# Optimization experiments

Hardware: AMD Instinct MI355X
Metric: run time of the kernel (lower is better)

The kernel has to match this reference:

```python
import jax, jax.numpy as jnp
import numpy as np

EPS = 1e-12

def l2norm(x):
    return x / jnp.maximum(jnp.linalg.norm(x, axis=-1, keepdims=True), EPS)

def setup_inputs() -> dict:
    key = jax.random.key(0)
    ks = jax.random.split(key, 10)
    B, N, Din, D, P, C = 2, 32768, 768, 512, 16, 2
    return {
        "x_s": jax.random.normal(ks[0], (B, N, Din), jnp.float32),
        "coord_s": jax.random.uniform(ks[1], (B, N, 2), jnp.float32),
        "x_l": jax.random.normal(ks[2], (B, N, Din), jnp.float32),
        "coord_l": jax.random.uniform(ks[3], (B, N, 2), jnp.float32),
        "W_proj": jax.random.normal(ks[4], (Din, D), jnp.float32) / np.sqrt(Din),
        "b_proj": jax.random.normal(ks[5], (D,), jnp.float32) * 0.01,
        "prototypes": jax.random.normal(ks[6], (P, D), jnp.float32),
        "text_low": l2norm(jax.random.normal(ks[7], (C, D), jnp.float32)),
        "text_high": l2norm(jax.random.normal(ks[8], (C, D), jnp.float32)),
        "label": jax.random.randint(ks[9], (B,), 0, C, jnp.int64),
    }

def forward_project(x, W, b):
    # Linear projection to hidden size, then L2 normalize (matches visual.forward_project + F.normalize)
    return l2norm(jnp.einsum('bni,id->bnd', x, W) + b)

def attention_pool(feats, prototypes):
    # feats: [B,N,D], prototypes: [P,D]
    D = feats.shape[-1]
    p = l2norm(prototypes)
    scores = jnp.einsum('bnd,pd->bpn', feats, p) / jnp.sqrt(jnp.asarray(D, feats.dtype))
    w = jax.nn.softmax(scores, axis=-1)                  # [B,P,N]
    attended = jnp.einsum('bpn,bnd->bpd', w, feats)       # [B,P,D]
    return l2norm(attended.mean(axis=1))                  # [B,D]

def reference(x_s, coord_s, x_l, coord_l, W_proj, b_proj, prototypes, text_low, text_high, label):
    x_s_proj = forward_project(x_s, W_proj, b_proj)
    x_l_proj = forward_project(x_l, W_proj, b_proj)
    feat_low = attention_pool(x_s_proj, prototypes)
    feat_high = attention_pool(x_l_proj, prototypes)
    logits = feat_low @ text_low.T + feat_high @ text_high.T   # [B,C]
    logp = jax.nn.log_softmax(logits, axis=-1)
    loss = -jnp.mean(jnp.take_along_axis(logp, label[:, None], axis=1))
    Y_prob = jax.nn.softmax(logits, axis=1)
    Y_hat = jnp.argmax(Y_prob, axis=1)
    return Y_prob, Y_hat, loss
```

## Files before the change

### kernel.cpp

```cpp
#include <hip/hip_runtime.h>
#include <hip/hip_bf16.h>
#include <math.h>

#define BB   2
#define NN   32768
#define DIN  768
#define DD   512
#define PP   16
#define MTOT (BB*NN)
#define MALL (2*MTOT)
#define NCHUNK 128
#define CHUNK  (NN/NCHUNK)
#define SCALE_INV_SQRT_D 0.04419417382415922f

typedef unsigned short u16;
typedef __attribute__((ext_vector_type(8))) short bf16x8;
typedef __attribute__((ext_vector_type(4))) float f32x4;

#define MFMA(a,b,c) __builtin_amdgcn_mfma_f32_16x16x32_bf16((a),(b),(c),0,0,0)

__device__ __forceinline__ unsigned pack2bf(float a, float b) {
  union { float f; unsigned u; } x{a}, y{b};
  unsigned ra = (x.u + 0x7FFFu + ((x.u >> 16) & 1u)) >> 16;
  unsigned rb = (y.u + 0x7FFFu + ((y.u >> 16) & 1u)) >> 16;
  return ra | (rb << 16);
}
__device__ __forceinline__ unsigned cvt2(float a, float b) {
  union { __hip_bfloat162 h; unsigned u; } x;
  x.h = __float22bfloat162_rn(make_float2(a, b));
  return x.u;
}
__device__ __forceinline__ u16 f2bf(float a) {
  union { float f; unsigned u; } x{a};
  return (u16)((x.u + 0x7FFFu + ((x.u >> 16) & 1u)) >> 16);
}
__device__ __forceinline__ float bf2f(u16 u) {
  union { unsigned u; float f; } x; x.u = ((unsigned)u) << 16; return x.f;
}

__device__ __forceinline__ float block_reduce_sum_256(float v, float* sred) {
  #pragma unroll
  for (int off = 32; off; off >>= 1) v += __shfl_down(v, off);
  const int lane = threadIdx.x & 63, w = threadIdx.x >> 6;
  if (lane == 0) sred[w] = v;
  __syncthreads();
  float r = sred[0] + sred[1] + sred[2] + sred[3];
  __syncthreads();
  return r;
}

__global__ __launch_bounds__(64) void pre_kernel(
    const float* __restrict__ W, const float* __restrict__ prot,
    uint4* __restrict__ Bf, uint4* __restrict__ pnb) {
  const int bid = blockIdx.x;
  const int lane = threadIdx.x;
  if (bid < 768) {
    const int nf = bid / 24, ks = bid % 24;
    const int n = nf*16 + (lane & 15);
    const int kb = ks*32 + (lane >> 4)*8;
    unsigned r0 = pack2bf(W[(size_t)(kb+0)*DD + n], W[(size_t)(kb+1)*DD + n]);
    unsigned r1 = pack2bf(W[(size_t)(kb+2)*DD + n], W[(size_t)(kb+3)*DD + n]);
    unsigned r2 = pack2bf(W[(size_t)(kb+4)*DD + n], W[(size_t)(kb+5)*DD + n]);
    unsigned r3 = pack2bf(W[(size_t)(kb+6)*DD + n], W[(size_t)(kb+7)*DD + n]);
    Bf[(size_t)bid*64 + lane] = make_uint4(r0, r1, r2, r3);
    return;
  }
  const int ks = bid - 768;
  const int p = lane & 15, seg = lane >> 4;
  float ssq = 0.f;
  for (int d = seg*128; d < seg*128 + 128; d += 4) {
    float4 v = *(const float4*)&prot[p*DD + d];
    ssq += v.x*v.x + v.y*v.y + v.z*v.z + v.w*v.w;
  }
  ssq += __shfl_xor(ssq, 16);
  ssq += __shfl_xor(ssq, 32);
  const float rnp = 1.f / fmaxf(sqrtf(ssq), 1e-12f);
  const int kb = ks*32 + seg*8;
  float v[8];
  #pragma unroll
  for (int j = 0; j < 8; ++j) v[j] = prot[p*DD + kb + j] * rnp;
  pnb[ks*64 + lane] = make_uint4(pack2bf(v[0],v[1]), pack2bf(v[2],v[3]),
                                 pack2bf(v[4],v[5]), pack2bf(v[6],v[7]));
}

__global__ __launch_bounds__(1024, 4) void gemm_kernel(
    const float* __restrict__ Xs, const float* __restrict__ Xl,
    const uint4* __restrict__ Bf, const float* __restrict__ bias,
    u16* __restrict__ proj, float* __restrict__ rnormb) {
  __shared__ __align__(16) unsigned char lds[163840];
  const int t = threadIdx.x, lane = t & 63, wid = t >> 6;
  const int wm = wid >> 3, wn = wid & 7;
  const int cl = lane & 15, cg = lane >> 4;
  const int m0g = blockIdx.x * 128;
  const float* Xb = (m0g < MTOT) ? Xs : Xl;
  const int m0l = m0g & (MTOT - 1);
  const int r = t >> 3, k8g = (t & 7) * 8;
  const float* gA = Xb + (size_t)(m0l + r) * DIN + k8g;
  const int aksl = k8g >> 5, acg = (k8g >> 3) & 3;
  const int awoff = ((r >> 4) * 2 + aksl) * 1024 + acg * 256
                  + (((r & 15) ^ ((acg << 1) | aksl)) << 4);

  f32x4 acc[4][4] = {};

#define STAGE_B(ktx, buf) \
  { _Pragma("unroll") \
    for (int q_ = 0; q_ < 4; ++q_) { \
      const int c_ = q_*16 + wid; \
      const uint4* src_ = Bf + ((size_t)((c_>>1)*24 + (ktx)*2 + (c_&1)))*64 + lane; \
      __builtin_amdgcn_global_load_lds( \
          (const __attribute__((address_space(1))) void*)src_, \
          (__attribute__((address_space(3))) void*)(lds + 32768 + (buf)*65536 + c_*1024 + lane*16), \
          16, 0, 0); \
    } }

  {
    STAGE_B(0, 0);
    float4 a0 = *(const float4*)gA;
    float4 a1 = *(const float4*)(gA + 4);
    *(uint4*)(lds + awoff) = make_uint4(cvt2(a0.x,a0.y), cvt2(a0.z,a0.w),
                                        cvt2(a1.x,a1.y), cvt2(a1.z,a1.w));
    __syncthreads();
  }
  for (int kt = 0; kt < 12; ++kt) {
    const int cur = kt & 1;
    float4 a0, a1;
    if (kt < 11) {
      STAGE_B(kt + 1, cur ^ 1);
      a0 = *(const float4*)(gA + (kt + 1) * 64);
      a1 = *(const float4*)(gA + (kt + 1) * 64 + 4);
    }
    #pragma unroll
    for (int ksl = 0; ksl < 2; ++ksl) {
      bf16x8 af[4], bfr[4];
      #pragma unroll
      for (int i = 0; i < 4; ++i)
        af[i] = *(const bf16x8*)(lds + cur*16384 + ((wm*4 + i)*2 + ksl)*1024 + cg*256
                                     + ((cl ^ ((cg << 1) | ksl)) << 4));
      #pragma unroll
      for (int j = 0; j < 4; ++j)
        bfr[j] = *(const bf16x8*)(lds + 32768 + cur*65536
                                      + ((wn*4 + j)*2 + ksl)*1024 + lane*16);
      #pragma unroll
      for (int i = 0; i < 4; ++i)
        #pragma unroll
        for (int j = 0; j < 4; ++j)
          acc[i][j] = MFMA(af[i], bfr[j], acc[i][j]);
    }
    if (kt < 11) {
      *(uint4*)(lds + (cur^1)*16384 + awoff) =
          make_uint4(cvt2(a0.x,a0.y), cvt2(a0.z,a0.w),
                     cvt2(a1.x,a1.y), cvt2(a1.z,a1.w));
    }
    __syncthreads();
  }
#undef STAGE_B
  float* ssqred = (float*)lds;
  float bv[4];
  #pragma unroll
  for (int j = 0; j < 4; ++j) bv[j] = bias[wn*64 + j*16 + cl];
  #pragma unroll
  for (int i = 0; i < 4; ++i) {
    #pragma unroll
    for (int rr = 0; rr < 4; ++rr) {
      const int rowl = wm*64 + i*16 + cg*4 + rr;
      u16* pr = proj + (size_t)(m0g + rowl) * DD + wn*64 + cl;
      float sq = 0.f;
      #pragma unroll
      for (int j = 0; j < 4; ++j) {
        float val = acc[i][j][rr] + bv[j];
        pr[j*16] = f2bf(val);
        sq += val * val;
      }
      sq += __shfl_xor(sq, 1); sq += __shfl_xor(sq, 2);
      sq += __shfl_xor(sq, 4); sq += __shfl_xor(sq, 8);
      if (cl == 0) ssqred[rowl*8 + wn] = sq;
    }
  }
  __syncthreads();
  if (t < 128) {
    float ss = 0.f;
    #pragma unroll
    for (int w = 0; w < 8; ++w) ss += ssqred[t*8 + w];
    rnormb[m0g + t] = 1.f / fmaxf(sqrtf(ss), 1e-12f);
  }
}

__global__ __launch_bounds__(256) void scores_kernel(
    const u16* __restrict__ proj, const uint4* __restrict__ pnb,
    const float* __restrict__ rnormb, u16* __restrict__ wbufe,
    float* __restrict__ espart) {
  __shared__ float esp[4][16];
  __shared__ u16 sbuf[128][18];
  const int t = threadIdx.x, lane = t & 63, wave = t >> 6;
  const int cl = lane & 15, cg = lane >> 4;
  bf16x8 pf[16];
  #pragma unroll
  for (int ks = 0; ks < 16; ++ks) pf[ks] = *(const bf16x8*)(pnb + ks*64 + lane);
  const int row0b = blockIdx.x * 128;
  float esum = 0.f;
  #pragma unroll
  for (int rg = 0; rg < 2; ++rg) {
    const int row0 = row0b + wave*32 + rg*16;
    f32x4 sacc = {0.f, 0.f, 0.f, 0.f};
    #pragma unroll
    for (int ks = 0; ks < 16; ++ks) {
      bf16x8 af = *(const bf16x8*)(proj + (size_t)(row0 + cl)*DD + ks*32 + cg*8);
      sacc = MFMA(af, pf[ks], sacc);
    }
    #pragma unroll
    for (int rr = 0; rr < 4; ++rr) {
      const int grow = row0 + cg*4 + rr;
      const float sc = sacc[rr] * rnormb[grow] * SCALE_INV_SQRT_D;
      const float e = expf(sc);
      esum += e;
      sbuf[wave*32 + rg*16 + cg*4 + rr][cl] = f2bf(e);
    }
  }
  esum += __shfl_xor(esum, 16);
  esum += __shfl_xor(esum, 32);
  if (lane < 16) esp[wave][lane] = esum;
  __syncthreads();
  if (t < 16)
    espart[(size_t)blockIdx.x * PP + t] = esp[0][t] + esp[1][t] + esp[2][t] + esp[3][t];
  {
    const int p = t >> 4, i8 = (t & 15) * 8;
    const int sbp = row0b >> 15, nb0 = row0b & (NN - 1);
    u16 tmp[8];
    #pragma unroll
    for (int k = 0; k < 8; ++k) tmp[k] = sbuf[i8 + k][p];
    *(uint4*)&wbufe[(size_t)(sbp*PP + p) * NN + nb0 + i8] = *(const uint4*)tmp;
  }
}

__global__ __launch_bounds__(256) void isum_kernel(const float* __restrict__ espart,
                                                   float* __restrict__ iSrow) {
  __shared__ float sred[4];
  const int bid = blockIdx.x, sbp = bid >> 4, p = bid & 15;
  const int t = threadIdx.x;
  float s = espart[(size_t)(sbp*256 + t)*PP + p];
  s = block_reduce_sum_256(s, sred);
  if (t == 0) iSrow[bid] = 1.f / s;
}

__global__ __launch_bounds__(256) void attended_kernel(
    const u16* __restrict__ proj, const u16* __restrict__ wbufe,
    const float* __restrict__ rnormb, const float* __restrict__ iSrow,
    float* __restrict__ part) {
  __shared__ float wl[CHUNK];
  __shared__ float iSl[PP];
  const int sb = blockIdx.y, cid = blockIdx.x, t = threadIdx.x;
  const int nbase = cid * CHUNK;
  if (t < PP) iSl[t] = iSrow[sb*PP + t];
  __syncthreads();
  if (t < CHUNK) {
    const int n = nbase + t;
    float s = 0.f;
    #pragma unroll
    for (int p = 0; p < PP; ++p)
      s += bf2f(wbufe[(size_t)(sb*PP + p)*NN + n]) * iSl[p];
    wl[t] = s * rnormb[sb*NN + n] * (1.f / PP);
  }
  __syncthreads();
  float a0 = 0.f, a1 = 0.f;
  const u16* pb = proj + ((size_t)sb * NN + nbase) * DD + 2*t;
  #pragma unroll 8
  for (int n = 0; n < CHUNK; ++n) {
    unsigned uu = *(const unsigned*)(pb + (size_t)n * DD);
    float w = wl[n];
    a0 += w * bf2f((u16)uu);
    a1 += w * bf2f((u16)(uu >> 16));
  }
  *(float2*)&part[((size_t)(sb*NCHUNK + cid))*DD + 2*t] = make_float2(a0, a1);
}

__global__ __launch_bounds__(256) void featred_kernel(
    const float* __restrict__ part, float* __restrict__ fraw) {
  __shared__ float red[2][128];
  const int sb = blockIdx.y, d0 = blockIdx.x * 128, t = threadIdx.x;
  const int dl = t & 127, half = t >> 7;
  float s = 0.f;
  for (int c = half*64; c < half*64 + 64; ++c)
    s += part[((size_t)(sb*NCHUNK + c))*DD + d0 + dl];
  red[half][dl] = s;
  __syncthreads();
  if (t < 128) fraw[sb*DD + d0 + t] = red[0][t] + red[1][t];
}

__global__ __launch_bounds__(256) void final_kernel(
    const float* __restrict__ fraw, const float* __restrict__ textL,
    const float* __restrict__ textH, const int* __restrict__ label,
    float* __restrict__ out) {
  __shared__ float sred[4];
  const int t = threadIdx.x;
  const float* frawL = fraw;
  const float* frawH = fraw + 2*DD;
  float invL[2], invH[2];
  #pragma unroll
  for (int b = 0; b < 2; ++b) {
    float v = 0.f;
    for (int d = t; d < DD; d += 256) { float x = frawL[b*DD + d]; v += x*x; }
    float ss = block_reduce_sum_256(v, sred);
    invL[b] = 1.f / fmaxf(sqrtf(ss), 1e-12f);
    v = 0.f;
    for (int d = t; d < DD; d += 256) { float x = frawH[b*DD + d]; v += x*x; }
    ss = block_reduce_sum_256(v, sred);
    invH[b] = 1.f / fmaxf(sqrtf(ss), 1e-12f);
  }
  float lg[2][2];
  #pragma unroll
  for (int b = 0; b < 2; ++b)
    #pragma unroll
    for (int c = 0; c < 2; ++c) {
      float v = 0.f;
      for (int d = t; d < DD; d += 256)
        v += frawL[b*DD + d] * invL[b] * textL[c*DD + d]
           + frawH[b*DD + d] * invH[b] * textH[c*DD + d];
      lg[b][c] = block_reduce_sum_256(v, sred);
    }
  if (t == 0) {
    float loss = 0.f;
    #pragma unroll
    for (int b = 0; b < 2; ++b) {
      const float m  = fmaxf(lg[b][0], lg[b][1]);
      const float lse = m + logf(expf(lg[b][0]-m) + expf(lg[b][1]-m));
      out[b*2+0] = expf(lg[b][0]-lse); out[b*2+1] = expf(lg[b][1]-lse);
      out[4+b] = (lg[b][1] > lg[b][0]) ? 1.f : 0.f;
      loss += -(lg[b][label[b]] - lse);
    }
    out[6] = loss * 0.5f;
  }
}

extern "C" void kernel_launch(void* const* d_in, const int* in_sizes, int n_in,
                              void* d_out, int out_size, void* d_ws, size_t ws_size,
                              hipStream_t stream) {
  (void)in_sizes; (void)n_in; (void)out_size; (void)ws_size;
  const float* x_s  = (const float*)d_in[0];
  const float* x_l  = (const float*)d_in[2];
  const float* Wp   = (const float*)d_in[4];
  const float* bp   = (const float*)d_in[5];
  const float* prot = (const float*)d_in[6];
  const float* tL   = (const float*)d_in[7];
  const float* tH   = (const float*)d_in[8];
  const int*   label= (const int*)d_in[9];
  float* out = (float*)d_out;

  unsigned char* w8 = (unsigned char*)d_ws;
  u16*   proj   = (u16*)  (w8);
  u16*   wbufe  = (u16*)  (w8 + 134217728);
  float* part   = (float*)(w8 + 138412032);
  float* rnormb = (float*)(w8 + 139460608);
  float* espart = (float*)(w8 + 139984896);
  float* iSrow  = (float*)(w8 + 140050432);
  uint4* Bf     = (uint4*)(w8 + 140051456);
  uint4* pnb    = (uint4*)(w8 + 140837888);
  float* fraw   = (float*)(w8 + 140854272);

  pre_kernel<<<784, 64, 0, stream>>>(Wp, prot, Bf, pnb);
  gemm_kernel<<<MALL/128, 1024, 0, stream>>>(x_s, x_l, Bf, bp, proj, rnormb);
  scores_kernel<<<MALL/128, 256, 0, stream>>>(proj, pnb, rnormb, wbufe, espart);
  isum_kernel<<<64, 256, 0, stream>>>(espart, iSrow);
  attended_kernel<<<dim3(NCHUNK, 4), 256, 0, stream>>>(proj, wbufe, rnormb, iSrow, part);
  featred_kernel<<<dim3(4, 4), 256, 0, stream>>>(part, fraw);
  final_kernel<<<1, 256, 0, stream>>>(fraw, tL, tH, label, out);
}
```

Measured before the change: 218.5 us.

## Split GEMM main loop into half-K stages with finer-grained waits and MFMA priority

Restructures the projection GEMM's K loop so the B-tile prefetch is issued in two halves interleaved with compute on the two K sub-slices. The single __syncthreads per iteration becomes explicit vmcnt/lgkmcnt waits plus s_barrier, so outstanding global loads can stay in flight across the first half of compute. s_setprio raises wave priority around the MFMA bursts, and the last iteration is peeled to drop the conditionals. The hand-written waitcnt counts depend on the exact instruction ordering the compiler emits and could cause races if that ordering changes.

```diff
diff --git a/kernel.cpp b/kernel.cpp
--- a/kernel.cpp
+++ b/kernel.cpp
@@ -102,58 +102,72 @@
 
   f32x4 acc[4][4] = {};
 
-#define STAGE_B(ktx, buf) \
+#define STAGE_BH(ktx, buf, h) \
   { _Pragma("unroll") \
-    for (int q_ = 0; q_ < 4; ++q_) { \
-      const int c_ = q_*16 + wid; \
-      const uint4* src_ = Bf + ((size_t)((c_>>1)*24 + (ktx)*2 + (c_&1)))*64 + lane; \
+    for (int q_ = 0; q_ < 2; ++q_) { \
+      const int nf_ = q_*16 + wid; \
+      const uint4* src_ = Bf + ((size_t)(nf_*24 + (ktx)*2 + (h)))*64 + lane; \
       __builtin_amdgcn_global_load_lds( \
           (const __attribute__((address_space(1))) void*)src_, \
-          (__attribute__((address_space(3))) void*)(lds + 32768 + (buf)*65536 + c_*1024 + lane*16), \
+          (__attribute__((address_space(3))) void*)(lds + 32768 + (buf)*65536 + (nf_*2 + (h))*1024 + lane*16), \
           16, 0, 0); \
     } }
 
+#define COMPUTE_HALF(cur, h) \
+  { bf16x8 af_[4], bfr_[4]; \
+    _Pragma("unroll") \
+    for (int i_ = 0; i_ < 4; ++i_) \
+      af_[i_] = *(const bf16x8*)(lds + (cur)*16384 + ((wm*4 + i_)*2 + (h))*1024 + cg*256 \
+                                     + ((cl ^ ((cg << 1) | (h))) << 4)); \
+    _Pragma("unroll") \
+    for (int j_ = 0; j_ < 4; ++j_) \
+      bfr_[j_] = *(const bf16x8*)(lds + 32768 + (cur)*65536 \
+                                      + ((wn*4 + j_)*2 + (h))*1024 + lane*16); \
+    __builtin_amdgcn_s_setprio(1); \
+    _Pragma("unroll") \
+    for (int i_ = 0; i_ < 4; ++i_) \
+      _Pragma("unroll") \
+      for (int j_ = 0; j_ < 4; ++j_) \
+        acc[i_][j_] = MFMA(af_[i_], bfr_[j_], acc[i_][j_]); \
+    __builtin_amdgcn_s_setprio(0); }
+
+#define A_WRITE(buf, va0, va1) \
+  *(uint4*)(lds + (buf)*16384 + awoff) = make_uint4( \
+      cvt2((va0).x,(va0).y), cvt2((va0).z,(va0).w), \
+      cvt2((va1).x,(va1).y), cvt2((va1).z,(va1).w));
+
   {
-    STAGE_B(0, 0);
     float4 a0 = *(const float4*)gA;
     float4 a1 = *(const float4*)(gA + 4);
-    *(uint4*)(lds + awoff) = make_uint4(cvt2(a0.x,a0.y), cvt2(a0.z,a0.w),
-                                        cvt2(a1.x,a1.y), cvt2(a1.z,a1.w));
-    __syncthreads();
-  }
-  for (int kt = 0; kt < 12; ++kt) {
+    STAGE_BH(0, 0, 0);
+    STAGE_BH(0, 0, 1);
+    A_WRITE(0, a0, a1);
+    asm volatile("s_waitcnt vmcnt(0) lgkmcnt(0)" ::: "memory");
+    __builtin_amdgcn_s_barrier();
+  }
+  for (int kt = 0; kt < 11; ++kt) {
     const int cur = kt & 1;
-    float4 a0, a1;
-    if (kt < 11) {
-      STAGE_B(kt + 1, cur ^ 1);
-      a0 = *(const float4*)(gA + (kt + 1) * 64);
-      a1 = *(const float4*)(gA + (kt + 1) * 64 + 4);
-    }
-    #pragma unroll
-    for (int ksl = 0; ksl < 2; ++ksl) {
-      bf16x8 af[4], bfr[4];
-      #pragma unroll
-      for (int i = 0; i < 4; ++i)
-        af[i] = *(const bf16x8*)(lds + cur*16384 + ((wm*4 + i)*2 + ksl)*1024 + cg*256
-                                     + ((cl ^ ((cg << 1) | ksl)) << 4));
-      #pragma unroll
-      for (int j = 0; j < 4; ++j)
-        bfr[j] = *(const bf16x8*)(lds + 32768 + cur*65536
-                                      + ((wn*4 + j)*2 + ksl)*1024 + lane*16);
-      #pragma unroll
-      for (int i = 0; i < 4; ++i)
-        #pragma unroll
-        for (int j = 0; j < 4; ++j)
-          acc[i][j] = MFMA(af[i], bfr[j], acc[i][j]);
-    }
-    if (kt < 11) {
-      *(uint4*)(lds + (cur^1)*16384 + awoff) =
-          make_uint4(cvt2(a0.x,a0.y), cvt2(a0.z,a0.w),
-                     cvt2(a1.x,a1.y), cvt2(a1.z,a1.w));
-    }
-    __syncthreads();
-  }
-#undef STAGE_B
+    float4 a0 = *(const float4*)(gA + (kt + 1) * 64);
+    float4 a1 = *(const float4*)(gA + (kt + 1) * 64 + 4);
+    STAGE_BH(kt + 1, cur ^ 1, 0);
+    COMPUTE_HALF(cur, 0);
+    asm volatile("s_waitcnt vmcnt(4)" ::: "memory");
+    __builtin_amdgcn_s_barrier();
+    STAGE_BH(kt + 1, cur ^ 1, 1);
+    COMPUTE_HALF(cur, 1);
+    A_WRITE(cur ^ 1, a0, a1);
+    asm volatile("s_waitcnt vmcnt(2) lgkmcnt(0)" ::: "memory");
+    __builtin_amdgcn_s_barrier();
+  }
+  COMPUTE_HALF(1, 0);
+  asm volatile("s_waitcnt vmcnt(0)" ::: "memory");
+  __builtin_amdgcn_s_barrier();
+  COMPUTE_HALF(1, 1);
+  asm volatile("s_waitcnt lgkmcnt(0)" ::: "memory");
+  __builtin_amdgcn_s_barrier();
+#undef STAGE_BH
+#undef COMPUTE_HALF
+#undef A_WRITE
   float* ssqred = (float*)lds;
   float bv[4];
   #pragma unroll
```

Measured after the change: 229.2 us. 4.9% more time.

## Split GEMM into 128x128 tiles with swizzled grid and deferred row norm

Applied to the files above, without the earlier changes.

The projection GEMM moves from one 1024-thread block per 128 rows covering all 512 columns to 256-thread blocks computing 128x128 tiles. The block index is swizzled so neighbouring blocks share A rows. The 160KB double-buffered LDS is replaced by a single 32KB buffer, which allows more blocks per CU but drops the load/compute overlap. Because each block now sees only a quarter of the columns, it writes per-tile partial sums of squares, and the scores kernel combines them into the reciprocal row norm. The A tile (fp32 input converted to bf16) is now read and converted four times, once per column tile.

```diff
diff --git a/kernel.cpp b/kernel.cpp
--- a/kernel.cpp
+++ b/kernel.cpp
@@ -83,87 +83,81 @@
                                  pack2bf(v[4],v[5]), pack2bf(v[6],v[7]));
 }
 
-__global__ __launch_bounds__(1024, 4) void gemm_kernel(
+__global__ __launch_bounds__(256, 4) void gemm_kernel(
     const float* __restrict__ Xs, const float* __restrict__ Xl,
     const uint4* __restrict__ Bf, const float* __restrict__ bias,
-    u16* __restrict__ proj, float* __restrict__ rnormb) {
-  __shared__ __align__(16) unsigned char lds[163840];
+    u16* __restrict__ proj, float* __restrict__ ssqp4) {
+  __shared__ __align__(16) unsigned char lds[32768];
   const int t = threadIdx.x, lane = t & 63, wid = t >> 6;
-  const int wm = wid >> 3, wn = wid & 7;
+  const int wm = wid >> 1, wn = wid & 1;
   const int cl = lane & 15, cg = lane >> 4;
-  const int m0g = blockIdx.x * 128;
+  const int id = blockIdx.x;
+  const int swz = (id & 7) * 512 + (id >> 3);
+  const int mb = swz >> 2, nb = swz & 3;
+  const int m0g = mb * 128, n0 = nb * 128;
   const float* Xb = (m0g < MTOT) ? Xs : Xl;
   const int m0l = m0g & (MTOT - 1);
-  const int r = t >> 3, k8g = (t & 7) * 8;
-  const float* gA = Xb + (size_t)(m0l + r) * DIN + k8g;
-  const int aksl = k8g >> 5, acg = (k8g >> 3) & 3;
-  const int awoff = ((r >> 4) * 2 + aksl) * 1024 + acg * 256
-                  + (((r & 15) ^ ((acg << 1) | aksl)) << 4);
+  const int r = t >> 1, kh = t & 1;
+  const float* gA = Xb + (size_t)(m0l + r) * DIN + kh * 32;
+  int awoff[4];
+  #pragma unroll
+  for (int q = 0; q < 4; ++q)
+    awoff[q] = ((r >> 4) * 2 + kh) * 1024 + q * 256
+             + (((r & 15) ^ ((q << 1) | kh)) << 4);
 
   f32x4 acc[4][4] = {};
 
-#define STAGE_B(ktx, buf) \
-  { _Pragma("unroll") \
-    for (int q_ = 0; q_ < 4; ++q_) { \
-      const int c_ = q_*16 + wid; \
-      const uint4* src_ = Bf + ((size_t)((c_>>1)*24 + (ktx)*2 + (c_&1)))*64 + lane; \
-      __builtin_amdgcn_global_load_lds( \
-          (const __attribute__((address_space(1))) void*)src_, \
-          (__attribute__((address_space(3))) void*)(lds + 32768 + (buf)*65536 + c_*1024 + lane*16), \
-          16, 0, 0); \
-    } }
-
-  {
-    STAGE_B(0, 0);
-    float4 a0 = *(const float4*)gA;
-    float4 a1 = *(const float4*)(gA + 4);
-    *(uint4*)(lds + awoff) = make_uint4(cvt2(a0.x,a0.y), cvt2(a0.z,a0.w),
-                                        cvt2(a1.x,a1.y), cvt2(a1.z,a1.w));
+  for (int kt = 0; kt < 12; ++kt) {
+    #pragma unroll
+    for (int q = 0; q < 4; ++q) {
+      const int c = q * 4 + wid;
+      const uint4* src = Bf + ((size_t)((nb * 8 + (c >> 1)) * 24 + kt * 2 + (c & 1))) * 64 + lane;
+      __builtin_amdgcn_global_load_lds(
+          (const __attribute__((address_space(1))) void*)src,
+          (__attribute__((address_space(3))) void*)(lds + 16384 + c * 1024 + lane * 16),
+          16, 0, 0);
+    }
+    const float* gAk = gA + kt * 64;
+    #pragma unroll
+    for (int h = 0; h < 2; ++h) {
+      float4 b0 = *(const float4*)(gAk + h*16);
+      float4 b1 = *(const float4*)(gAk + h*16 + 4);
+      float4 b2 = *(const float4*)(gAk + h*16 + 8);
+      float4 b3 = *(const float4*)(gAk + h*16 + 12);
+      *(uint4*)(lds + awoff[2*h]) =
+          make_uint4(cvt2(b0.x,b0.y), cvt2(b0.z,b0.w), cvt2(b1.x,b1.y), cvt2(b1.z,b1.w));
+      *(uint4*)(lds + awoff[2*h+1]) =
+          make_uint4(cvt2(b2.x,b2.y), cvt2(b2.z,b2.w), cvt2(b3.x,b3.y), cvt2(b3.z,b3.w));
+    }
     __syncthreads();
-  }
-  for (int kt = 0; kt < 12; ++kt) {
-    const int cur = kt & 1;
-    float4 a0, a1;
-    if (kt < 11) {
-      STAGE_B(kt + 1, cur ^ 1);
-      a0 = *(const float4*)(gA + (kt + 1) * 64);
-      a1 = *(const float4*)(gA + (kt + 1) * 64 + 4);
-    }
     #pragma unroll
     for (int ksl = 0; ksl < 2; ++ksl) {
       bf16x8 af[4], bfr[4];
       #pragma unroll
       for (int i = 0; i < 4; ++i)
-        af[i] = *(const bf16x8*)(lds + cur*16384 + ((wm*4 + i)*2 + ksl)*1024 + cg*256
+        af[i] = *(const bf16x8*)(lds + ((wm*4 + i)*2 + ksl)*1024 + cg*256
                                      + ((cl ^ ((cg << 1) | ksl)) << 4));
       #pragma unroll
       for (int j = 0; j < 4; ++j)
-        bfr[j] = *(const bf16x8*)(lds + 32768 + cur*65536
-                                      + ((wn*4 + j)*2 + ksl)*1024 + lane*16);
+        bfr[j] = *(const bf16x8*)(lds + 16384 + ((wn*4 + j)*2 + ksl)*1024 + lane*16);
       #pragma unroll
       for (int i = 0; i < 4; ++i)
         #pragma unroll
         for (int j = 0; j < 4; ++j)
           acc[i][j] = MFMA(af[i], bfr[j], acc[i][j]);
     }
-    if (kt < 11) {
-      *(uint4*)(lds + (cur^1)*16384 + awoff) =
-          make_uint4(cvt2(a0.x,a0.y), cvt2(a0.z,a0.w),
-                     cvt2(a1.x,a1.y), cvt2(a1.z,a1.w));
-    }
     __syncthreads();
   }
-#undef STAGE_B
   float* ssqred = (float*)lds;
   float bv[4];
   #pragma unroll
-  for (int j = 0; j < 4; ++j) bv[j] = bias[wn*64 + j*16 + cl];
+  for (int j = 0; j < 4; ++j) bv[j] = bias[n0 + wn*64 + j*16 + cl];
   #pragma unroll
   for (int i = 0; i < 4; ++i) {
     #pragma unroll
     for (int rr = 0; rr < 4; ++rr) {
       const int rowl = wm*64 + i*16 + cg*4 + rr;
-      u16* pr = proj + (size_t)(m0g + rowl) * DD + wn*64 + cl;
+      u16* pr = proj + (size_t)(m0g + rowl) * DD + n0 + wn*64 + cl;
       float sq = 0.f;
       #pragma unroll
       for (int j = 0; j < 4; ++j) {
@@ -173,22 +167,17 @@
       }
       sq += __shfl_xor(sq, 1); sq += __shfl_xor(sq, 2);
       sq += __shfl_xor(sq, 4); sq += __shfl_xor(sq, 8);
-      if (cl == 0) ssqred[rowl*8 + wn] = sq;
-    }
-  }
-  __syncthreads();
-  if (t < 128) {
-    float ss = 0.f;
-    #pragma unroll
-    for (int w = 0; w < 8; ++w) ss += ssqred[t*8 + w];
-    rnormb[m0g + t] = 1.f / fmaxf(sqrtf(ss), 1e-12f);
-  }
+      if (cl == 0) ssqred[rowl*2 + wn] = sq;
+    }
+  }
+  __syncthreads();
+  if (t < 128) ssqp4[(size_t)(m0g + t) * 4 + nb] = ssqred[t*2] + ssqred[t*2 + 1];
 }
 
 __global__ __launch_bounds__(256) void scores_kernel(
     const u16* __restrict__ proj, const uint4* __restrict__ pnb,
-    const float* __restrict__ rnormb, u16* __restrict__ wbufe,
-    float* __restrict__ espart) {
+    const float* __restrict__ ssqp4, float* __restrict__ rnormb,
+    u16* __restrict__ wbufe, float* __restrict__ espart) {
   __shared__ float esp[4][16];
   __shared__ u16 sbuf[128][18];
   const int t = threadIdx.x, lane = t & 63, wave = t >> 6;
@@ -210,7 +199,10 @@
     #pragma unroll
     for (int rr = 0; rr < 4; ++rr) {
       const int grow = row0 + cg*4 + rr;
-      const float sc = sacc[rr] * rnormb[grow] * SCALE_INV_SQRT_D;
+      const float4 sp = *(const float4*)&ssqp4[(size_t)grow * 4];
+      const float rn = 1.f / fmaxf(sqrtf(sp.x + sp.y + sp.z + sp.w), 1e-12f);
+      if (cl == 0) rnormb[grow] = rn;
+      const float sc = sacc[rr] * rn * SCALE_INV_SQRT_D;
       const float e = expf(sc);
       esum += e;
       sbuf[wave*32 + rg*16 + cg*4 + rr][cl] = f2bf(e);
@@ -348,17 +340,18 @@
   unsigned char* w8 = (unsigned char*)d_ws;
   u16*   proj   = (u16*)  (w8);
   u16*   wbufe  = (u16*)  (w8 + 134217728);
+  float* ssqp4  = (float*)(w8 + 138412032);
   float* part   = (float*)(w8 + 138412032);
-  float* rnormb = (float*)(w8 + 139460608);
-  float* espart = (float*)(w8 + 139984896);
-  float* iSrow  = (float*)(w8 + 140050432);
-  uint4* Bf     = (uint4*)(w8 + 140051456);
-  uint4* pnb    = (uint4*)(w8 + 140837888);
-  float* fraw   = (float*)(w8 + 140854272);
+  float* rnormb = (float*)(w8 + 140509184);
+  float* espart = (float*)(w8 + 141033472);
+  float* iSrow  = (float*)(w8 + 141099008);
+  uint4* Bf     = (uint4*)(w8 + 141100032);
+  uint4* pnb    = (uint4*)(w8 + 141886464);
+  float* fraw   = (float*)(w8 + 141902848);
 
   pre_kernel<<<784, 64, 0, stream>>>(Wp, prot, Bf, pnb);
-  gemm_kernel<<<MALL/128, 1024, 0, stream>>>(x_s, x_l, Bf, bp, proj, rnormb);
-  scores_kernel<<<MALL/128, 256, 0, stream>>>(proj, pnb, rnormb, wbufe, espart);
+  gemm_kernel<<<4096, 256, 0, stream>>>(x_s, x_l, Bf, bp, proj, ssqp4);
+  scores_kernel<<<MALL/128, 256, 0, stream>>>(proj, pnb, ssqp4, rnormb, wbufe, espart);
   isum_kernel<<<64, 256, 0, stream>>>(espart, iSrow);
   attended_kernel<<<dim3(NCHUNK, 4), 256, 0, stream>>>(proj, wbufe, rnormb, iSrow, part);
   featred_kernel<<<dim3(4, 4), 256, 0, stream>>>(part, fraw);
```

Result: slower. 529.8 us (+142.4%).
